# Optimization experiments

Hardware: AMD Instinct MI355X
Metric: run time of the kernel (lower is better)

Reference implementation:

```python
import jax, jax.numpy as jnp
import numpy as np

B, N, C, H = 8, 1024, 768, 12
HD = C // H  # 64
SCALE = HD ** -0.5
T = 4
N_HALF = T // 2  # loop body with attention runs N_HALF times, V accumulates T times


def setup_inputs() -> dict:
    key = jax.random.key(0)
    ks = jax.random.split(key, 8)
    s = 0.02
    return {
        "x": jax.random.normal(ks[0], (B, N, C), jnp.float32),
        "Wqkv": jax.random.normal(ks[1], (3 * C, C), jnp.float32) * s,
        "Wfc1": jax.random.normal(ks[2], (HD, HD), jnp.float32) * s,
        "bfc1": jax.random.normal(ks[3], (HD,), jnp.float32) * s,
        "Wfc2": jax.random.normal(ks[4], (HD, HD), jnp.float32) * s,
        "bfc2": jax.random.normal(ks[5], (HD,), jnp.float32) * s,
        "Wproj": jax.random.normal(ks[6], (C, C), jnp.float32) * s,
        "bproj": jax.random.normal(ks[7], (C,), jnp.float32) * s,
    }


def reference(x, Wqkv, Wfc1, bfc1, Wfc2, bfc2, Wproj, bproj):
    b, n, c = x.shape
    # qkv projection (no bias), split into per-head q,k,v: [B,H,N,hd]
    qkv = (x @ Wqkv.T).reshape(b, n, 3, H, HD).transpose(2, 0, 3, 1, 4)
    q, k, v = qkv[0], qkv[1], qkv[2]
    # Loop body is stateless per timestep: first N_HALF steps each add the same
    # att_spk; all T steps add the same relu(v). Compute once, scale by counts.
    Q_spk = jax.nn.relu(q) @ Wfc1.T + bfc1  # [B,H,N,hd]
    K_spk = jax.nn.relu(k) @ Wfc2.T + bfc2  # [B,H,N,hd]
    att_spk = jax.nn.relu(jnp.einsum("bhqd,bhkd->bhqk", Q_spk, K_spk) * SCALE)
    att_rec = att_spk * float(N_HALF)   # accumulated over t < T/2
    V_rec = jax.nn.relu(v) * float(T)   # accumulated over all T steps
    att = jax.nn.softmax(att_rec, axis=-1)
    out = jnp.einsum("bhqk,bhkd->bhqd", att, V_rec)  # [B,H,N,hd]
    out = out.transpose(0, 2, 1, 3).reshape(b, n, c)
    return out @ Wproj.T + bproj
```

## Files before the change

kernel.cpp:

```cpp
#include <hip/hip_runtime.h>
#include <hip/hip_bf16.h>
#include <stdint.h>
#include <math.h>

#define BB   8
#define NN_  1024
#define CC   768
#define HH   12
#define HDD  64

typedef __attribute__((ext_vector_type(8))) short bf16x8;
typedef __attribute__((ext_vector_type(4))) float f32x4;
typedef __attribute__((ext_vector_type(16))) float f32x16;
typedef __attribute__((ext_vector_type(4))) float f32x4v;
typedef __attribute__((ext_vector_type(4))) unsigned short u16x4;

union FragU { unsigned int u[4]; bf16x8 b; };

__device__ __forceinline__ unsigned short f2bf(float f) {
    union { float f; unsigned int u; } v; v.f = f;
    unsigned int r = v.u + 0x7fffu + ((v.u >> 16) & 1u);
    return (unsigned short)(r >> 16);
}

#define CVTPK(d_, a_, b_) asm("v_cvt_pk_bf16_f32 %0, %1, %2" : "=v"(d_) : "v"(a_), "v"(b_))
#define SWAP32(a_, b_) asm("v_permlane32_swap_b32 %0, %1" : "+v"(a_), "+v"(b_))

#define GLDS(g_, l_) __builtin_amdgcn_global_load_lds( \
    (const __attribute__((address_space(1))) void*)(g_), \
    (__attribute__((address_space(3))) void*)(l_), 16, 0, 0)

#define MKFRAGS(P_, F0_, F1_) do {                                             \
    unsigned int c0,c1,c2,c3,c4,c5,c6,c7;                                      \
    CVTPK(c0, P_[0],  P_[1]);  CVTPK(c1, P_[2],  P_[3]);                       \
    CVTPK(c2, P_[4],  P_[5]);  CVTPK(c3, P_[6],  P_[7]);                       \
    CVTPK(c4, P_[8],  P_[9]);  CVTPK(c5, P_[10], P_[11]);                      \
    CVTPK(c6, P_[12], P_[13]); CVTPK(c7, P_[14], P_[15]);                      \
    SWAP32(c0, c2); SWAP32(c1, c3); SWAP32(c4, c6); SWAP32(c5, c7);            \
    FragU fu0_, fu1_;                                                          \
    fu0_.u[0]=c0; fu0_.u[1]=c1; fu0_.u[2]=c2; fu0_.u[3]=c3;                    \
    fu1_.u[0]=c4; fu1_.u[1]=c5; fu1_.u[2]=c6; fu1_.u[3]=c7;                    \
    F0_ = fu0_.b; F1_ = fu1_.b;                                                \
} while (0)

#define CVT_N0 1572864
#define CVT_N1 2015232
#define CVT_N2 2162688
#define CVT_N3 2163712
#define CVT_N4 2164736
__global__ void cvt_all(const float* __restrict__ x, const float* __restrict__ wqkv,
                        const float* __restrict__ wproj, const float* __restrict__ wf1,
                        const float* __restrict__ wf2,
                        unsigned short* __restrict__ xb, unsigned short* __restrict__ wqkvb,
                        unsigned short* __restrict__ wprojb, unsigned short* __restrict__ wf1b,
                        unsigned short* __restrict__ wf2b) {
    int i = blockIdx.x * blockDim.x + threadIdx.x;
    int stride = gridDim.x * blockDim.x;
    for (; i < CVT_N4; i += stride) {
        const f32x4v* src; u16x4* dst; int off;
        if (i < CVT_N0)      { src = (const f32x4v*)x;     dst = (u16x4*)xb;     off = i; }
        else if (i < CVT_N1) { src = (const f32x4v*)wqkv;  dst = (u16x4*)wqkvb;  off = i - CVT_N0; }
        else if (i < CVT_N2) { src = (const f32x4v*)wproj; dst = (u16x4*)wprojb; off = i - CVT_N1; }
        else if (i < CVT_N3) { src = (const f32x4v*)wf1;   dst = (u16x4*)wf1b;   off = i - CVT_N2; }
        else                 { src = (const f32x4v*)wf2;   dst = (u16x4*)wf2b;   off = i - CVT_N3; }
        f32x4v v = src[off];
        u16x4 o;
        o.x = f2bf(v.x); o.y = f2bf(v.y); o.z = f2bf(v.z); o.w = f2bf(v.w);
        dst[off] = o;
    }
}

__global__ __launch_bounds__(512, 2)
void qkv_spk_gemm(const unsigned short* __restrict__ X,
                  const unsigned short* __restrict__ Wqkv,
                  const unsigned short* __restrict__ Wf1,
                  const unsigned short* __restrict__ Wf2,
                  const float* __restrict__ bf1,
                  const float* __restrict__ bf2,
                  unsigned short* __restrict__ Rq,
                  unsigned short* __restrict__ Rk,
                  unsigned short* __restrict__ VT) {
    __shared__ short sA[3][8192];
    __shared__ short sB[3][4096];

    const int t    = threadIdx.x;
    const int wid  = t >> 6;
    const int lane = t & 63;
    const int l31  = lane & 31;
    const int hi5  = lane >> 5;
    const int fw   = wid >> 1;
    const int wn   = wid & 1;

    const int bid  = (int)blockIdx.x;
    const int lbid = (bid & 7) * 72 + (bid >> 3);
    const int bx   = lbid & 63;
    const int by   = lbid >> 6;
    const int F0   = by * 256;
    const int T0   = bx * 128;

#define STG(bi_, kt_) do {                                                     \
    _Pragma("unroll")                                                          \
    for (int i = 0; i < 2; i++) {                                              \
        int li_ = i * 512 + t;                                                 \
        int dr_ = li_ >> 3;                                                    \
        int u_  = (li_ & 7) ^ (dr_ & 7);                                       \
        GLDS(Wqkv + (size_t)(F0 + dr_ * 2 + (u_ >> 2)) * 768 + (kt_) * 32 + (u_ & 3) * 8, \
             &sA[bi_][li_ * 8]);                                               \
    }                                                                          \
    {                                                                          \
        int dr_ = t >> 3;                                                      \
        int u_  = (t & 7) ^ (dr_ & 7);                                         \
        GLDS(X + (size_t)(T0 + dr_ * 2 + (u_ >> 2)) * 768 + (kt_) * 32 + (u_ & 3) * 8, \
             &sB[bi_][t * 8]);                                                 \
    }                                                                          \
} while (0)

    f32x16 acc[2][2];
#pragma unroll
    for (int fb = 0; fb < 2; fb++)
#pragma unroll
        for (int tb = 0; tb < 2; tb++)
#pragma unroll
            for (int r = 0; r < 16; r++) acc[fb][tb][r] = 0.f;

#define PH(bc_, kt_) do {                                                      \
    if ((kt_) + 2 < 24) STG(((bc_) + 2) % 3, (kt_) + 2);                       \
    const char* ab_ = (const char*)sA[bc_];                                    \
    const char* bb_ = (const char*)sB[bc_];                                    \
    bf16x8 wf_[2][2], xf_[2][2];                                               \
    _Pragma("unroll")                                                          \
    for (int fb = 0; fb < 2; fb++) {                                           \
        int r_ = fw * 64 + fb * 32 + l31;                                      \
        int dr_ = r_ >> 1;                                                     \
        _Pragma("unroll")                                                      \
        for (int ks = 0; ks < 2; ks++)                                         \
            wf_[fb][ks] = *(const bf16x8*)(ab_ + dr_ * 128 +                   \
                ((((r_ & 1) * 4 + ks * 2 + hi5) ^ (dr_ & 7)) << 4));           \
    }                                                                          \
    _Pragma("unroll")                                                          \
    for (int tb = 0; tb < 2; tb++) {                                           \
        int r_ = wn * 64 + tb * 32 + l31;                                      \
        int dr_ = r_ >> 1;                                                     \
        _Pragma("unroll")                                                      \
        for (int ks = 0; ks < 2; ks++)                                         \
            xf_[tb][ks] = *(const bf16x8*)(bb_ + dr_ * 128 +                   \
                ((((r_ & 1) * 4 + ks * 2 + hi5) ^ (dr_ & 7)) << 4));           \
    }                                                                          \
    __builtin_amdgcn_s_setprio(1);                                             \
    _Pragma("unroll")                                                          \
    for (int ks = 0; ks < 2; ks++)                                             \
        _Pragma("unroll")                                                      \
        for (int fb = 0; fb < 2; fb++)                                         \
            _Pragma("unroll")                                                  \
            for (int tb = 0; tb < 2; tb++)                                     \
                acc[fb][tb] = __builtin_amdgcn_mfma_f32_32x32x16_bf16(         \
                    wf_[fb][ks], xf_[tb][ks], acc[fb][tb], 0, 0, 0);           \
    __builtin_amdgcn_s_setprio(0);                                             \
    asm volatile("s_waitcnt vmcnt(3)" ::: "memory");                           \
    __builtin_amdgcn_s_barrier();                                              \
} while (0)

    STG(0, 0);
    STG(1, 1);
    asm volatile("s_waitcnt vmcnt(3)" ::: "memory");
    __builtin_amdgcn_s_barrier();

#pragma unroll 1
    for (int kt3 = 0; kt3 < 24; kt3 += 3) {
        PH(0, kt3);
        PH(1, kt3 + 1);
        PH(2, kt3 + 2);
    }
#undef PH
#undef STG

    const int fbase = F0 + fw * 64;
    const int p  = fbase / 768;
    const int hh = (fbase - p * 768) >> 6;
    const int tok0 = T0 + wn * 64;
    const int b  = tok0 >> 10;
    const int n0 = tok0 & 1023;
    const int crow0 = 4 * hi5;

    if (p == 2) {
        const size_t vtb = ((size_t)(b * HH + hh)) * HDD * NN_;
#pragma unroll
        for (int fb = 0; fb < 2; fb++)
#pragma unroll
            for (int tb = 0; tb < 2; tb++)
#pragma unroll
                for (int r = 0; r < 16; r++) {
                    int d = fb * 32 + (r & 3) + 8 * (r >> 2) + crow0;
                    int n = n0 + tb * 32 + l31;
                    VT[vtb + (size_t)d * NN_ + n] = f2bf(4.f * fmaxf(acc[fb][tb][r], 0.f));
                }
    } else {
        const unsigned short* Wf = p ? Wf2 : Wf1;
        const float* bfp = p ? bf2 : bf1;
        unsigned short* R = p ? Rk : Rq;
        bf16x8 wfr[2][4];
#pragma unroll
        for (int dh = 0; dh < 2; dh++)
#pragma unroll
            for (int ks = 0; ks < 4; ks++)
                wfr[dh][ks] = *(const bf16x8*)&Wf[(size_t)(dh * 32 + l31) * HDD + ks * 16 + hi5 * 8];
        float bv0 = bfp[l31], bv1 = bfp[32 + l31];
        const size_t qkb = ((size_t)(b * HH + hh)) * NN_ * HDD;
#pragma unroll
        for (int tb = 0; tb < 2; tb++) {
            float pv0[16], pv1[16];
#pragma unroll
            for (int r = 0; r < 16; r++) {
                pv0[r] = fmaxf(acc[0][tb][r], 0.f);
                pv1[r] = fmaxf(acc[1][tb][r], 0.f);
            }
            bf16x8 pa0, pa1, pa2, pa3;
            MKFRAGS(pv0, pa0, pa1);
            MKFRAGS(pv1, pa2, pa3);
            f32x16 D0, D1;
#pragma unroll
            for (int r = 0; r < 16; r++) { D0[r] = 0.f; D1[r] = 0.f; }
            D0 = __builtin_amdgcn_mfma_f32_32x32x16_bf16(pa0, wfr[0][0], D0, 0, 0, 0);
            D0 = __builtin_amdgcn_mfma_f32_32x32x16_bf16(pa1, wfr[0][1], D0, 0, 0, 0);
            D0 = __builtin_amdgcn_mfma_f32_32x32x16_bf16(pa2, wfr[0][2], D0, 0, 0, 0);
            D0 = __builtin_amdgcn_mfma_f32_32x32x16_bf16(pa3, wfr[0][3], D0, 0, 0, 0);
            D1 = __builtin_amdgcn_mfma_f32_32x32x16_bf16(pa0, wfr[1][0], D1, 0, 0, 0);
            D1 = __builtin_amdgcn_mfma_f32_32x32x16_bf16(pa1, wfr[1][1], D1, 0, 0, 0);
            D1 = __builtin_amdgcn_mfma_f32_32x32x16_bf16(pa2, wfr[1][2], D1, 0, 0, 0);
            D1 = __builtin_amdgcn_mfma_f32_32x32x16_bf16(pa3, wfr[1][3], D1, 0, 0, 0);
#pragma unroll
            for (int r = 0; r < 16; r++) {
                int n = n0 + tb * 32 + (r & 3) + 8 * (r >> 2) + crow0;
                size_t rowb = qkb + (size_t)n * HDD;
                R[rowb + l31]      = f2bf(D0[r] + bv0);
                R[rowb + 32 + l31] = f2bf(D1[r] + bv1);
            }
        }
    }
}

__global__ __launch_bounds__(256, 2)
void attn_kernel(const unsigned short* __restrict__ Q,
                 const unsigned short* __restrict__ Kx,
                 const unsigned short* __restrict__ VT,
                 unsigned short* __restrict__ AO) {
    __shared__ short sK[2][64 * 64];
    __shared__ short sV[2][64 * 64];
    __shared__ float sinv[4][32];

    const int t    = threadIdx.x;
    const int lane = t & 63;
    const int wid  = t >> 6;
    const int l31  = lane & 31;
    const int hi5  = lane >> 5;

    const int bid = (int)blockIdx.x;
    const int lbid = (bid & 7) * 96 + (bid >> 3);
    const int bh = lbid >> 3;
    const int qt = lbid & 7;
    const int b = bh / HH, h = bh - b * HH;

    const unsigned short* Qs = Q  + (size_t)bh * NN_ * HDD;
    const unsigned short* Ks = Kx + (size_t)bh * NN_ * HDD;
    const unsigned short* Vt = VT + (size_t)bh * HDD * NN_;
    const int q0 = qt * 128 + wid * 32;

    bf16x8 qf[4];
#pragma unroll
    for (int ds = 0; ds < 4; ds++)
        qf[ds] = *(const bf16x8*)&Qs[(size_t)(q0 + l31) * HDD + ds * 16 + hi5 * 8];

    f32x16 O0, O1;
#pragma unroll
    for (int r = 0; r < 16; r++) { O0[r] = 0.f; O1[r] = 0.f; }
    float sumacc = 0.f;

    const int srow = t >> 3;
    const int sslot = t & 7;
    const int dstoff = ((t & 192)) * 8;

#define STAGE(buf_, kt_) do {                                                  \
    _Pragma("unroll")                                                          \
    for (int i = 0; i < 2; i++) {                                              \
        int row_ = srow + i * 32;                                              \
        int sl_  = (sslot ^ (row_ & 7)) << 3;                                  \
        const unsigned short* gk_ = Ks + (size_t)((kt_) * 64 + row_) * HDD + sl_; \
        const unsigned short* gv_ = Vt + (size_t)row_ * NN_ + (kt_) * 64 + sl_;   \
        GLDS(gk_, &sK[buf_][i * 2048 + dstoff]);                               \
        GLDS(gv_, &sV[buf_][i * 2048 + dstoff]);                               \
    }                                                                          \
} while (0)

    STAGE(0, 0);
    __syncthreads();

    int buf = 0;
    for (int kt = 0; kt < 16; ++kt) {
        if (kt < 15) STAGE(buf ^ 1, kt + 1);

        const char* kbase = (const char*)&sK[buf][0];
        const char* vbase = (const char*)&sV[buf][0];

        bf16x8 vbf[4][2];
#pragma unroll
        for (int ks = 0; ks < 4; ks++)
#pragma unroll
            for (int dt = 0; dt < 2; dt++) {
                int d = dt * 32 + l31;
                vbf[ks][dt] = *(const bf16x8*)(vbase + d * 128 +
                               ((ks * 32 + hi5 * 16) ^ ((d & 7) << 4)));
            }
        bf16x8 ka[2][4];
#pragma unroll
        for (int kt2 = 0; kt2 < 2; kt2++)
#pragma unroll
            for (int ds = 0; ds < 4; ds++) {
                int kk = kt2 * 32 + l31;
                ka[kt2][ds] = *(const bf16x8*)(kbase + kk * 128 +
                               ((ds * 32 + hi5 * 16) ^ ((kk & 7) << 4)));
            }

        f32x16 S0, S1;
#pragma unroll
        for (int r = 0; r < 16; r++) { S0[r] = 0.f; S1[r] = 0.f; }
#pragma unroll
        for (int ds = 0; ds < 4; ds++) {
            S0 = __builtin_amdgcn_mfma_f32_32x32x16_bf16(ka[0][ds], qf[ds], S0, 0, 0, 0);
            S1 = __builtin_amdgcn_mfma_f32_32x32x16_bf16(ka[1][ds], qf[ds], S1, 0, 0, 0);
        }

        float p0[16], p1[16];
#pragma unroll
        for (int r = 0; r < 16; r++) {
            p0[r] = exp2f(0.36067376f * fmaxf(S0[r], 0.f));
            p1[r] = exp2f(0.36067376f * fmaxf(S1[r], 0.f));
        }
        float s0 = 0.f, s1 = 0.f;
#pragma unroll
        for (int r = 0; r < 16; r++) { s0 += p0[r]; s1 += p1[r]; }
        sumacc += s0 + s1;

        bf16x8 paf0, paf1, paf2, paf3;
        MKFRAGS(p0, paf0, paf1);
        MKFRAGS(p1, paf2, paf3);

        O0 = __builtin_amdgcn_mfma_f32_32x32x16_bf16(paf0, vbf[0][0], O0, 0, 0, 0);
        O1 = __builtin_amdgcn_mfma_f32_32x32x16_bf16(paf0, vbf[0][1], O1, 0, 0, 0);
        O0 = __builtin_amdgcn_mfma_f32_32x32x16_bf16(paf1, vbf[1][0], O0, 0, 0, 0);
        O1 = __builtin_amdgcn_mfma_f32_32x32x16_bf16(paf1, vbf[1][1], O1, 0, 0, 0);
        O0 = __builtin_amdgcn_mfma_f32_32x32x16_bf16(paf2, vbf[2][0], O0, 0, 0, 0);
        O1 = __builtin_amdgcn_mfma_f32_32x32x16_bf16(paf2, vbf[2][1], O1, 0, 0, 0);
        O0 = __builtin_amdgcn_mfma_f32_32x32x16_bf16(paf3, vbf[3][0], O0, 0, 0, 0);
        O1 = __builtin_amdgcn_mfma_f32_32x32x16_bf16(paf3, vbf[3][1], O1, 0, 0, 0);

        __syncthreads();
        buf ^= 1;
    }
#undef STAGE

    float stot = sumacc + __shfl_xor(sumacc, 32, 64);
    float inv = 1.f / stot;
    if (l31 == lane) sinv[wid][l31] = inv;
    __syncthreads();

#pragma unroll
    for (int r = 0; r < 16; r++) {
        int qloc = (r & 3) + 8 * (r >> 2) + 4 * hi5;
        float iv = sinv[wid][qloc];
        size_t row = (size_t)(b * NN_ + q0 + qloc) * CC + h * HDD;
        AO[row + l31]      = f2bf(O0[r] * iv);
        AO[row + 32 + l31] = f2bf(O1[r] * iv);
    }
}

__global__ __launch_bounds__(256)
void proj_gemm(const unsigned short* __restrict__ A,
               const unsigned short* __restrict__ Bt,
               const float* __restrict__ bias,
               float* __restrict__ Out) {
    __shared__ short sA[128 * 32];
    __shared__ short sB[128 * 32];
    const int K = 768;
    const int lane = threadIdx.x & 63;
    const int wid  = threadIdx.x >> 6;
    const int wr = wid >> 1, wc = wid & 1;
    const int brow = blockIdx.x * 128;
    const int bcol = blockIdx.y * 128;
    const int t = threadIdx.x;

    f32x4 acc[4][4];
#pragma unroll
    for (int m = 0; m < 4; m++)
#pragma unroll
        for (int n = 0; n < 4; n++) acc[m][n] = (f32x4){0.f, 0.f, 0.f, 0.f};

    for (int k0 = 0; k0 < K; k0 += 32) {
#pragma unroll
        for (int i = 0; i < 2; i++) {
            int tt  = i * 256 + t;
            int row = tt >> 2;
            int kc  = (tt & 3) * 8;
            const unsigned short* ga = A  + (size_t)(brow + row) * K + k0 + kc;
            const unsigned short* gb = Bt + (size_t)(bcol + row) * K + k0 + kc;
            GLDS(ga, &sA[(i * 256 + wid * 64) * 8]);
            GLDS(gb, &sB[(i * 256 + wid * 64) * 8]);
        }
        __syncthreads();
        bf16x8 af[4], bfg[4];
#pragma unroll
        for (int m = 0; m < 4; m++) {
            int r = wr * 64 + m * 16 + (lane & 15);
            af[m] = *(const bf16x8*)&sA[r * 32 + (lane >> 4) * 8];
        }
#pragma unroll
        for (int n = 0; n < 4; n++) {
            int c = wc * 64 + n * 16 + (lane & 15);
            bfg[n] = *(const bf16x8*)&sB[c * 32 + (lane >> 4) * 8];
        }
#pragma unroll
        for (int m = 0; m < 4; m++)
#pragma unroll
            for (int n = 0; n < 4; n++)
                acc[m][n] = __builtin_amdgcn_mfma_f32_16x16x32_bf16(af[m], bfg[n], acc[m][n], 0, 0, 0);
        __syncthreads();
    }
#pragma unroll
    for (int m = 0; m < 4; m++)
#pragma unroll
        for (int n = 0; n < 4; n++) {
            int col = bcol + wc * 64 + n * 16 + (lane & 15);
            float bv = bias[col];
#pragma unroll
            for (int r = 0; r < 4; r++) {
                int row = brow + wr * 64 + m * 16 + (lane >> 4) * 4 + r;
                Out[(size_t)row * 768 + col] = acc[m][n][r] + bv;
            }
        }
}

extern "C" void kernel_launch(void* const* d_in, const int* in_sizes, int n_in,
                              void* d_out, int out_size, void* d_ws, size_t ws_size,
                              hipStream_t stream) {
    const float* x     = (const float*)d_in[0];
    const float* Wqkv  = (const float*)d_in[1];
    const float* Wfc1  = (const float*)d_in[2];
    const float* bfc1  = (const float*)d_in[3];
    const float* Wfc2  = (const float*)d_in[4];
    const float* bfc2  = (const float*)d_in[5];
    const float* Wproj = (const float*)d_in[6];
    const float* bproj = (const float*)d_in[7];
    float* out = (float*)d_out;

    char* ws = (char*)d_ws;
    const size_t SZ_XN = (size_t)8192 * 768 * 2;
    unsigned short* x_bf    = (unsigned short*)ws; ws += SZ_XN;
    unsigned short* wqkv_bf = (unsigned short*)ws; ws += (size_t)2304 * 768 * 2;
    unsigned short* wproj_bf= (unsigned short*)ws; ws += (size_t)768 * 768 * 2;
    unsigned short* wfc1_bf = (unsigned short*)ws; ws += 64 * 64 * 2;
    unsigned short* wfc2_bf = (unsigned short*)ws; ws += 64 * 64 * 2;
    unsigned short* Rq      = (unsigned short*)ws; ws += SZ_XN;
    unsigned short* Rk      = (unsigned short*)ws; ws += SZ_XN;
    unsigned short* VT      = (unsigned short*)ws; ws += SZ_XN;

    cvt_all<<<2048, 256, 0, stream>>>(x, Wqkv, Wproj, Wfc1, Wfc2,
                                      x_bf, wqkv_bf, wproj_bf, wfc1_bf, wfc2_bf);
    qkv_spk_gemm<<<576, 512, 0, stream>>>(x_bf, wqkv_bf, wfc1_bf, wfc2_bf,
                                          bfc1, bfc2, Rq, Rk, VT);
    attn_kernel<<<768, 256, 0, stream>>>(Rq, Rk, VT, x_bf);
    proj_gemm<<<dim3(64, 6), 256, 0, stream>>>(x_bf, wproj_bf, bproj, out);
}
```

Baseline: 137.6 us.

## Deepen QKV GEMM pipeline to four LDS stages with register double-buffering

The QKV projection GEMM main loop moves from a 3-stage to a 4-stage LDS ring and prefetches the next tile's fragments into a second register set while the current MFMAs run. This hides LDS read latency and global load latency behind the matrix ops. The larger LDS footprint forces occupancy down to one 512-thread block per CU, and launch bounds are lowered to match. Fewer resident waves may expose latency that two blocks previously covered.

```diff
diff --git a/kernel.cpp b/kernel.cpp
--- a/kernel.cpp
+++ b/kernel.cpp
@@ -70,7 +70,7 @@
     }
 }
 
-__global__ __launch_bounds__(512, 2)
+__global__ __launch_bounds__(512, 1)
 void qkv_spk_gemm(const unsigned short* __restrict__ X,
                   const unsigned short* __restrict__ Wqkv,
                   const unsigned short* __restrict__ Wf1,
@@ -80,8 +80,8 @@
                   unsigned short* __restrict__ Rq,
                   unsigned short* __restrict__ Rk,
                   unsigned short* __restrict__ VT) {
-    __shared__ short sA[3][8192];
-    __shared__ short sB[3][4096];
+    __shared__ short sA[4][8192];
+    __shared__ short sB[4][4096];
 
     const int t    = threadIdx.x;
     const int wid  = t >> 6;
@@ -123,18 +123,18 @@
 #pragma unroll
             for (int r = 0; r < 16; r++) acc[fb][tb][r] = 0.f;
 
-#define PH(bc_, kt_) do {                                                      \
-    if ((kt_) + 2 < 24) STG(((bc_) + 2) % 3, (kt_) + 2);                       \
+    bf16x8 wA[2][2], xA[2][2], wB[2][2], xB[2][2];
+
+#define RD(W_, X_, bc_) do {                                                   \
     const char* ab_ = (const char*)sA[bc_];                                    \
     const char* bb_ = (const char*)sB[bc_];                                    \
-    bf16x8 wf_[2][2], xf_[2][2];                                               \
     _Pragma("unroll")                                                          \
     for (int fb = 0; fb < 2; fb++) {                                           \
         int r_ = fw * 64 + fb * 32 + l31;                                      \
         int dr_ = r_ >> 1;                                                     \
         _Pragma("unroll")                                                      \
         for (int ks = 0; ks < 2; ks++)                                         \
-            wf_[fb][ks] = *(const bf16x8*)(ab_ + dr_ * 128 +                   \
+            W_[fb][ks] = *(const bf16x8*)(ab_ + dr_ * 128 +                    \
                 ((((r_ & 1) * 4 + ks * 2 + hi5) ^ (dr_ & 7)) << 4));           \
     }                                                                          \
     _Pragma("unroll")                                                          \
@@ -143,10 +143,12 @@
         int dr_ = r_ >> 1;                                                     \
         _Pragma("unroll")                                                      \
         for (int ks = 0; ks < 2; ks++)                                         \
-            xf_[tb][ks] = *(const bf16x8*)(bb_ + dr_ * 128 +                   \
+            X_[tb][ks] = *(const bf16x8*)(bb_ + dr_ * 128 +                    \
                 ((((r_ & 1) * 4 + ks * 2 + hi5) ^ (dr_ & 7)) << 4));           \
     }                                                                          \
-    __builtin_amdgcn_s_setprio(1);                                             \
+} while (0)
+
+#define MFMA8(W_, X_)                                                          \
     _Pragma("unroll")                                                          \
     for (int ks = 0; ks < 2; ks++)                                             \
         _Pragma("unroll")                                                      \
@@ -154,24 +156,40 @@
             _Pragma("unroll")                                                  \
             for (int tb = 0; tb < 2; tb++)                                     \
                 acc[fb][tb] = __builtin_amdgcn_mfma_f32_32x32x16_bf16(         \
-                    wf_[fb][ks], xf_[tb][ks], acc[fb][tb], 0, 0, 0);           \
+                    W_[fb][ks], X_[tb][ks], acc[fb][tb], 0, 0, 0)
+
+#define PH(CW_, CX_, NW_, NX_, rb_, sb_, t_, VM_) do {                         \
+    if ((t_) + 3 < 24) STG(sb_, (t_) + 3);                                     \
+    asm volatile("s_waitcnt vmcnt(" #VM_ ")" ::: "memory");                    \
+    __builtin_amdgcn_s_barrier();                                              \
+    if ((t_) + 1 < 24) RD(NW_, NX_, rb_);                                      \
+    __builtin_amdgcn_sched_barrier(0);                                         \
+    __builtin_amdgcn_s_setprio(1);                                             \
+    MFMA8(CW_, CX_);                                                           \
     __builtin_amdgcn_s_setprio(0);                                             \
-    asm volatile("s_waitcnt vmcnt(3)" ::: "memory");                           \
-    __builtin_amdgcn_s_barrier();                                              \
+    asm volatile("s_waitcnt lgkmcnt(0)" ::: "memory");                         \
 } while (0)
 
-    STG(0, 0);
-    STG(1, 1);
-    asm volatile("s_waitcnt vmcnt(3)" ::: "memory");
+    STG(0, 0); STG(1, 1); STG(2, 2);
+    asm volatile("s_waitcnt vmcnt(6)" ::: "memory");
     __builtin_amdgcn_s_barrier();
+    RD(wA, xA, 0);
+    asm volatile("s_waitcnt lgkmcnt(0)" ::: "memory");
 
 #pragma unroll 1
-    for (int kt3 = 0; kt3 < 24; kt3 += 3) {
-        PH(0, kt3);
-        PH(1, kt3 + 1);
-        PH(2, kt3 + 2);
-    }
+    for (int t4 = 0; t4 < 20; t4 += 4) {
+        PH(wA, xA, wB, xB, 1, 3, t4 + 0, 6);
+        PH(wB, xB, wA, xA, 2, 0, t4 + 1, 6);
+        PH(wA, xA, wB, xB, 3, 1, t4 + 2, 6);
+        PH(wB, xB, wA, xA, 0, 2, t4 + 3, 6);
+    }
+    PH(wA, xA, wB, xB, 1, 3, 20, 6);
+    PH(wB, xB, wA, xA, 2, 0, 21, 3);
+    PH(wA, xA, wB, xB, 3, 1, 22, 0);
+    PH(wB, xB, wA, xA, 0, 2, 23, 0);
 #undef PH
+#undef MFMA8
+#undef RD
 #undef STG
 
     const int fbase = F0 + fw * 64;
```

Result: no change. 137.8 us (+0.2%).
